# Kernel optimization log

Measured on AMD Instinct MI355X. Metric: run time of the kernel, lower is better.

## Reference

```python
import jax, jax.numpy as jnp
import numpy as np

N, B, D = 2048, 4, 2048   # seq_len, batch, embed_dim (sequence-first layout)
E = 2                     # expand_ratio
H = D // E                # number of heads
EPS = 1e-5


def setup_inputs() -> dict:
    key = jax.random.key(0)
    ks = jax.random.split(key, 3)
    x = jax.random.normal(ks[0], (N, B, D), dtype=jnp.float32)
    W_in = jax.random.normal(ks[1], (3 * D, D), dtype=jnp.float32) / np.sqrt(D).astype(np.float32)
    b_in = jnp.zeros((3 * D,), jnp.float32)
    W_out = jax.random.normal(ks[2], (D, D), dtype=jnp.float32) / np.sqrt(D).astype(np.float32)
    b_out = jnp.zeros((D,), jnp.float32)
    gamma = jnp.ones((D,), jnp.float32)
    beta = jnp.zeros((D,), jnp.float32)
    return {"x": x, "W_in": W_in, "b_in": b_in, "gamma": gamma, "beta": beta,
            "W_out": W_out, "b_out": b_out}


def _linear_scan(lam, u):
    # h_t = lam_t * h_{t-1} + u_t along time axis 0 (HgruRealFunction)
    def combine(c1, c2):
        a1, b1 = c1
        a2, b2 = c2
        return a1 * a2, a2 * b1 + b2
    _, h = jax.lax.associative_scan(combine, (lam, u), axis=0)
    return h


def _layernorm(x, gamma, beta):
    mu = jnp.mean(x, axis=-1, keepdims=True)
    var = jnp.var(x, axis=-1, keepdims=True)
    return (x - mu) * jax.lax.rsqrt(var + EPS) * gamma + beta


def reference(x, W_in, b_in, gamma, beta, W_out, b_out):
    n, b, d = x.shape
    feat = x @ W_in.T + b_in                       # (n,b,3d)
    inp, og, fg = jnp.split(feat, 3, axis=-1)
    inp = jax.nn.silu(inp)                         # act_fun = silu
    og = jax.nn.sigmoid(og)                        # uv_act_fun = sigmoid
    lam = jax.nn.sigmoid(fg)                       # lower_bound = 0 => lambda = sigmoid(F)

    inp = inp.reshape(n, b, H, E)
    og = og.reshape(n, b, H, E)
    lam = lam.reshape(n, b, H, E)

    # input = einsum('...hd,...he->...hde', 1-lambda, input)
    u = ((1.0 - lam)[..., :, None] * inp[..., None, :]).reshape(n, b, H * E * E)
    lam_f = jnp.broadcast_to(lam[..., :, None], (n, b, H, E, E)).reshape(n, b, H * E * E)

    s_fwd = _linear_scan(lam_f, u)
    s_rev = jnp.flip(_linear_scan(jnp.flip(lam_f, 0), jnp.flip(u, 0)), 0)
    s = (s_fwd + s_rev).reshape(n, b, H, E, E)

    o = jnp.einsum('nbhde,nbhd->nbhe', s, og).reshape(n, b, d)
    o = _layernorm(o, gamma, beta)
    return o @ W_out.T + b_out
```

## Files before the change

### kernel.cpp

```cpp
#include <hip/hip_runtime.h>
#include <hip/hip_bf16.h>

#define NSEQ 2048
#define NB   4
#define DIM  2048
#define HN   1024
#define FC   6144
#define MROWS 8192
#define CHUNKS 64
#define CLEN 32
#define NCH  4096

typedef __bf16 bf16x8_t __attribute__((ext_vector_type(8)));
typedef float  f32x4_t  __attribute__((ext_vector_type(4)));

__device__ __forceinline__ float sigm(float x){ return 1.f/(1.f + __expf(-x)); }
__device__ __forceinline__ float bflo(unsigned p){ return __uint_as_float(p << 16); }
__device__ __forceinline__ float bfhi(unsigned p){ return __uint_as_float(p & 0xffff0000u); }
__device__ __forceinline__ unsigned short f2bf(float f){
  union { __hip_bfloat16 h; unsigned short u; } cv;
  cv.h = __float2bfloat16(f);
  return cv.u;
}

__global__ __launch_bounds__(256) void cvt_bf16_4(const float4* __restrict__ in,
                                                  ushort4* __restrict__ out, int n4){
  int i = blockIdx.x * blockDim.x + threadIdx.x;
  int st = gridDim.x * blockDim.x;
  for (; i < n4; i += st){
    float4 v = in[i];
    ushort4 r;
    r.x = f2bf(v.x); r.y = f2bf(v.y); r.z = f2bf(v.z); r.w = f2bf(v.w);
    out[i] = r;
  }
}

__device__ __forceinline__ void gl_lds16(const void* g, void* l){
  __builtin_amdgcn_global_load_lds((const __attribute__((address_space(1))) void*)g,
                                   (__attribute__((address_space(3))) void*)l, 16, 0, 0);
}

template<int SLOT,int KSUB,int MH,bool VM, class SG>
__device__ __forceinline__ void do_phase(const __hip_bfloat16* smem,
    const int* aoff, const int* boff, bf16x8_t (&Bf)[4], f32x4_t (&acc)[8][4], SG&& sg){
  if (VM) asm volatile("s_waitcnt vmcnt(6)" ::: "memory");
  const __hip_bfloat16* base = smem + SLOT*32768 + KSUB*8192;
  bf16x8_t Af[4];
  #pragma unroll
  for (int mi = 0; mi < 4; ++mi)
    Af[mi] = *reinterpret_cast<const bf16x8_t*>(base + aoff[MH*4 + mi]);
  if (MH == 0){
    #pragma unroll
    for (int n = 0; n < 4; ++n)
      Bf[n] = *reinterpret_cast<const bf16x8_t*>(base + 16384 + boff[n]);
  }
  sg();
  __builtin_amdgcn_s_barrier();
  asm volatile("s_waitcnt lgkmcnt(0)" ::: "memory");
  __builtin_amdgcn_sched_barrier(0);
  __builtin_amdgcn_s_setprio(1);
  #pragma unroll
  for (int mi = 0; mi < 4; ++mi)
    #pragma unroll
    for (int n = 0; n < 4; ++n)
      acc[MH*4 + mi][n] =
        __builtin_amdgcn_mfma_f32_16x16x32_bf16(Af[mi], Bf[n], acc[MH*4 + mi][n], 0, 0, 0);
  __builtin_amdgcn_s_setprio(0);
  __builtin_amdgcn_s_barrier();
}

template <typename OutT>
__global__ __launch_bounds__(512, 2) void gemm256(const __hip_bfloat16* __restrict__ A,
                                                  const __hip_bfloat16* __restrict__ B,
                                                  const float* __restrict__ bias,
                                                  OutT* __restrict__ C,
                                                  int M, int N, int K, int nbx){
  __shared__ __align__(16) __hip_bfloat16 smem[65536];
  const int tid  = threadIdx.x;
  const int wave = tid >> 6, lane = tid & 63;

  const int cpx = gridDim.x >> 3;
  const int wg  = (blockIdx.x & 7) * cpx + (blockIdx.x >> 3);
  const int bx = wg % nbx, by = wg / nbx;
  const int m0 = by * 256, n0 = bx * 256;

  const int wr = wave >> 2, wc = wave & 3;
  const int r  = lane & 15, q = lane >> 4;
  const int NT = K >> 6;

  int aoff[8], boff[4];
  #pragma unroll
  for (int f = 0; f < 8; ++f){
    int R = wr*128 + (f>>2)*64 + (f&3)*16 + r;
    aoff[f] = (R>>1)*64 + (((((R&1)<<2) | q) ^ ((R>>1)&7)) << 3);
  }
  #pragma unroll
  for (int n = 0; n < 4; ++n){
    int R = wc*64 + n*16 + r;
    boff[n] = (R>>1)*64 + (((((R&1)<<2) | q) ^ ((R>>1)&7)) << 3);
  }

  auto stage_half = [&](int slot, int ab, int khalf, int ktile){
    if (ktile >= NT) return;
    const __hip_bfloat16* Base = ab ? B : A;
    const int t0 = ab ? n0 : m0;
    const int kc = ktile*64 + khalf*32;
    const int hb = slot*32768 + ab*16384 + khalf*8192;
    #pragma unroll
    for (int i = 0; i < 2; ++i){
      int g = i*512 + tid;
      int line = g >> 3, glp = g & 7;
      int glog = glp ^ (line & 7);
      int row = line*2 + (glog >> 2);
      int kg = glog & 3;
      gl_lds16(Base + (size_t)(t0 + row)*K + kc + kg*8, smem + hb + g*8);
    }
  };

  f32x4_t acc[8][4] = {};
  bf16x8_t Bf[4];

  stage_half(0,0,0, 0); stage_half(0,1,0, 0); stage_half(0,0,1, 0); stage_half(0,1,1, 0);
  stage_half(1,1,0, 1); stage_half(1,0,0, 1); stage_half(1,1,1, 1);
  asm volatile("s_waitcnt vmcnt(6)" ::: "memory");
  __builtin_amdgcn_s_barrier();

  for (int j = 0; j < NT/2; ++j){
    const int kb = 2*j;
    do_phase<0,0,0,true >(smem, aoff, boff, Bf, acc, [&]{ stage_half(1,0,1, kb+1); });
    do_phase<0,0,1,false>(smem, aoff, boff, Bf, acc, [&]{ stage_half(0,1,0, kb+2); });
    do_phase<0,1,0,true >(smem, aoff, boff, Bf, acc, [&]{ stage_half(0,0,0, kb+2); });
    do_phase<0,1,1,false>(smem, aoff, boff, Bf, acc, [&]{ stage_half(0,1,1, kb+2); });
    do_phase<1,0,0,true >(smem, aoff, boff, Bf, acc, [&]{ stage_half(0,0,1, kb+2); });
    do_phase<1,0,1,false>(smem, aoff, boff, Bf, acc, [&]{ stage_half(1,1,0, kb+3); });
    do_phase<1,1,0,true >(smem, aoff, boff, Bf, acc, [&]{ stage_half(1,0,0, kb+3); });
    do_phase<1,1,1,false>(smem, aoff, boff, Bf, acc, [&]{ stage_half(1,1,1, kb+3); });
  }

  #pragma unroll
  for (int fn = 0; fn < 4; ++fn){
    int col = n0 + wc*64 + fn*16 + r;
    float bv = bias[col];
    #pragma unroll
    for (int fm = 0; fm < 8; ++fm){
      int row0 = m0 + wr*128 + fm*16 + q*4;
      #pragma unroll
      for (int jj = 0; jj < 4; ++jj){
        float v = acc[fm][fn][jj] + bv;
        if constexpr (__is_same(OutT, float))
          C[(size_t)(row0 + jj)*N + col] = v;
        else
          C[(size_t)(row0 + jj)*N + col] = __float2bfloat16(v);
      }
    }
  }
}

struct SV { float l0, l1, u00, u01, u10, u11; };
__device__ __forceinline__ SV stepv(const unsigned* __restrict__ fp, int rowu){
  unsigned pi = fp[rowu];
  unsigned pf = fp[rowu + 2048];
  SV s;
  s.l0 = sigm(bflo(pf)); s.l1 = sigm(bfhi(pf));
  float i0 = bflo(pi), i1 = bfhi(pi);
  i0 *= sigm(i0); i1 *= sigm(i1);
  float a0 = 1.f - s.l0, a1 = 1.f - s.l1;
  s.u00 = a0*i0; s.u01 = a0*i1; s.u10 = a1*i0; s.u11 = a1*i1;
  return s;
}

__global__ __launch_bounds__(256) void scan_agg(const unsigned* __restrict__ feat,
    float* __restrict__ aggP, float4* __restrict__ aggHF, float4* __restrict__ aggHR){
  int ch = blockIdx.x*256 + threadIdx.x;
  int c  = blockIdx.y;
  int b = ch >> 10, h = ch & 1023;
  int base = b*3072 + h;
  int n0 = c*CLEN;
  float P0 = 1.f, P1 = 1.f;
  float f00=0,f01=0,f10=0,f11=0;
  for (int t = 0; t < CLEN; ++t){
    SV s = stepv(feat, (n0+t)*12288 + base);
    f00 = s.l0*f00 + s.u00; f01 = s.l0*f01 + s.u01;
    f10 = s.l1*f10 + s.u10; f11 = s.l1*f11 + s.u11;
    P0 *= s.l0; P1 *= s.l1;
  }
  float r00=0,r01=0,r10=0,r11=0;
  for (int t = CLEN-1; t >= 0; --t){
    SV s = stepv(feat, (n0+t)*12288 + base);
    r00 = s.l0*r00 + s.u00; r01 = s.l0*r01 + s.u01;
    r10 = s.l1*r10 + s.u10; r11 = s.l1*r11 + s.u11;
  }
  aggP[c*8192 + ch*2]     = P0;
  aggP[c*8192 + ch*2 + 1] = P1;
  aggHF[c*4096 + ch] = make_float4(f00,f01,f10,f11);
  aggHR[c*4096 + ch] = make_float4(r00,r01,r10,r11);
}

__global__ __launch_bounds__(256) void scan_carry(const float* __restrict__ aggP,
    const float* __restrict__ aggHF, const float* __restrict__ aggHR,
    float* __restrict__ cF, float* __restrict__ cR){
  int t  = blockIdx.x*256 + threadIdx.x;
  int pd = t >> 1;
  float s = 0.f;
  for (int c = 0; c < CHUNKS; ++c){
    cF[c*16384 + t] = s;
    s = aggP[c*8192 + pd]*s + aggHF[c*16384 + t];
  }
  s = 0.f;
  for (int c = CHUNKS-1; c >= 0; --c){
    cR[c*16384 + t] = s;
    s = aggP[c*8192 + pd]*s + aggHR[c*16384 + t];
  }
}

__global__ __launch_bounds__(256) void scan_fr(const unsigned* __restrict__ feat,
    const float4* __restrict__ cF, const float4* __restrict__ cR,
    float2* __restrict__ o){
  int ch = blockIdx.x*256 + threadIdx.x;
  int c  = blockIdx.y;
  int b = ch >> 10, h = ch & 1023;
  int base = b*3072 + h;
  float2 accv[CLEN];
  {
    float4 hv = cF[c*4096 + ch];
    float h00=hv.x, h01=hv.y, h10=hv.z, h11=hv.w;
    #pragma unroll
    for (int t = 0; t < CLEN; ++t){
      int rowu = (c*CLEN + t)*12288 + base;
      SV s = stepv(feat, rowu);
      h00 = s.l0*h00 + s.u00; h01 = s.l0*h01 + s.u01;
      h10 = s.l1*h10 + s.u10; h11 = s.l1*h11 + s.u11;
      unsigned po = feat[rowu + 1024];
      float g0 = sigm(bflo(po)), g1 = sigm(bfhi(po));
      accv[t] = make_float2(g0*h00 + g1*h10, g0*h01 + g1*h11);
    }
  }
  {
    float4 hv = cR[c*4096 + ch];
    float h00=hv.x, h01=hv.y, h10=hv.z, h11=hv.w;
    #pragma unroll
    for (int t = CLEN-1; t >= 0; --t){
      int rowu = (c*CLEN + t)*12288 + base;
      SV s = stepv(feat, rowu);
      h00 = s.l0*h00 + s.u00; h01 = s.l0*h01 + s.u01;
      h10 = s.l1*h10 + s.u10; h11 = s.l1*h11 + s.u11;
      unsigned po = feat[rowu + 1024];
      float g0 = sigm(bflo(po)), g1 = sigm(bfhi(po));
      accv[t].x += g0*h00 + g1*h10;
      accv[t].y += g0*h01 + g1*h11;
    }
  }
  #pragma unroll
  for (int t = 0; t < CLEN; ++t)
    o[((c*CLEN + t)*NB + b)*1024 + h] = accv[t];
}

__global__ __launch_bounds__(256) void layernorm_k(const float* __restrict__ o,
    const float* __restrict__ gamma, const float* __restrict__ beta,
    __hip_bfloat16* __restrict__ out){
  int row = blockIdx.x, t = threadIdx.x;
  const float4* x = (const float4*)(o + (size_t)row*DIM);
  float4 a = x[t], b = x[t + 256];
  float s  = (a.x + a.y) + (a.z + a.w) + (b.x + b.y) + (b.z + b.w);
  float ss = (a.x*a.x + a.y*a.y) + (a.z*a.z + a.w*a.w)
           + (b.x*b.x + b.y*b.y) + (b.z*b.z + b.w*b.w);
  #pragma unroll
  for (int off = 32; off > 0; off >>= 1){
    s  += __shfl_down(s, off);
    ss += __shfl_down(ss, off);
  }
  __shared__ float red[8];
  int wv = t >> 6, ln = t & 63;
  if (ln == 0){ red[wv] = s; red[4 + wv] = ss; }
  __syncthreads();
  float S  = (red[0] + red[1]) + (red[2] + red[3]);
  float SS = (red[4] + red[5]) + (red[6] + red[7]);
  float mu = S * (1.f/DIM);
  float rs = rsqrtf(SS * (1.f/DIM) - mu*mu + 1e-5f);
  const float4* gp = (const float4*)gamma;
  const float4* bp = (const float4*)beta;
  float4 g0 = gp[t], g1 = gp[t + 256], be0 = bp[t], be1 = bp[t + 256];
  ushort4* op = (ushort4*)(out + (size_t)row*DIM);
  ushort4 r0, r1;
  r0.x = f2bf((a.x - mu)*rs*g0.x + be0.x);
  r0.y = f2bf((a.y - mu)*rs*g0.y + be0.y);
  r0.z = f2bf((a.z - mu)*rs*g0.z + be0.z);
  r0.w = f2bf((a.w - mu)*rs*g0.w + be0.w);
  r1.x = f2bf((b.x - mu)*rs*g1.x + be1.x);
  r1.y = f2bf((b.y - mu)*rs*g1.y + be1.y);
  r1.z = f2bf((b.z - mu)*rs*g1.z + be1.z);
  r1.w = f2bf((b.w - mu)*rs*g1.w + be1.w);
  op[t] = r0; op[t + 256] = r1;
}

extern "C" void kernel_launch(void* const* d_in, const int* in_sizes, int n_in,
                              void* d_out, int out_size, void* d_ws, size_t ws_size,
                              hipStream_t stream){
  (void)in_sizes; (void)n_in; (void)out_size;
  const float* x     = (const float*)d_in[0];
  const float* W_in  = (const float*)d_in[1];
  const float* b_in  = (const float*)d_in[2];
  const float* gamma = (const float*)d_in[3];
  const float* beta  = (const float*)d_in[4];
  const float* W_out = (const float*)d_in[5];
  const float* b_out = (const float*)d_in[6];
  float* out = (float*)d_out;

  char* p = (char*)d_ws;
  auto carve = [&](size_t bytes) -> char* {
    char* r = p; p += (bytes + 255) & ~(size_t)255; return r;
  };
  __hip_bfloat16* feat = (__hip_bfloat16*)carve((size_t)MROWS*FC*2);
  char* U              = carve((size_t)MROWS*DIM*4);
  __hip_bfloat16* Wob  = (__hip_bfloat16*)carve((size_t)DIM*DIM*2);
  float* aggP  = (float*)carve((size_t)CHUNKS*8192*4);
  float* aggHF = (float*)carve((size_t)CHUNKS*16384*4);
  float* aggHR = (float*)carve((size_t)CHUNKS*16384*4);
  float* cF    = (float*)carve((size_t)CHUNKS*16384*4);
  float* cR    = (float*)carve((size_t)CHUNKS*16384*4);
  if ((size_t)(p - (char*)d_ws) > ws_size) return;

  __hip_bfloat16* xb  = (__hip_bfloat16*)U;
  __hip_bfloat16* Wib = (__hip_bfloat16*)(U + (size_t)MROWS*DIM*2);
  float* o            = (float*)U;
  __hip_bfloat16* oln = (__hip_bfloat16*)feat;

  cvt_bf16_4<<<2048, 256, 0, stream>>>((const float4*)x,     (ushort4*)xb,  MROWS*DIM/4);
  cvt_bf16_4<<<2048, 256, 0, stream>>>((const float4*)W_in,  (ushort4*)Wib, FC*DIM/4);
  cvt_bf16_4<<<1024, 256, 0, stream>>>((const float4*)W_out, (ushort4*)Wob, DIM*DIM/4);

  gemm256<__hip_bfloat16><<<768, 512, 0, stream>>>(xb, Wib, b_in, feat, MROWS, FC, 2048, FC/256);

  scan_agg  <<<dim3(NCH/256, CHUNKS), 256, 0, stream>>>((const unsigned*)feat, aggP, (float4*)aggHF, (float4*)aggHR);
  scan_carry<<<64, 256, 0, stream>>>(aggP, aggHF, aggHR, cF, cR);
  scan_fr   <<<dim3(NCH/256, CHUNKS), 256, 0, stream>>>((const unsigned*)feat, (const float4*)cF, (const float4*)cR, (float2*)o);

  layernorm_k<<<MROWS, 256, 0, stream>>>(o, gamma, beta, oln);

  gemm256<float><<<256, 512, 0, stream>>>(oln, Wob, b_out, out, MROWS, DIM, 2048, DIM/256);
}
```

Baseline: 479.8 us.

## Double-buffer LDS fragment reads to overlap with MFMA in GEMM phases

```diff
diff --git a/kernel.cpp b/kernel.cpp
--- a/kernel.cpp
+++ b/kernel.cpp
@@ -40,32 +40,35 @@
                                    (__attribute__((address_space(3))) void*)l, 16, 0, 0);
 }
 
-template<int SLOT,int KSUB,int MH,bool VM, class SG>
-__device__ __forceinline__ void do_phase(const __hip_bfloat16* smem,
-    const int* aoff, const int* boff, bf16x8_t (&Bf)[4], f32x4_t (&acc)[8][4], SG&& sg){
-  if (VM) asm volatile("s_waitcnt vmcnt(6)" ::: "memory");
-  const __hip_bfloat16* base = smem + SLOT*32768 + KSUB*8192;
-  bf16x8_t Af[4];
+template<int P, bool VM, class SG>
+__device__ __forceinline__ void phase(const __hip_bfloat16* smem,
+    const int (&aoff)[8], const int (&boff)[4],
+    bf16x8_t (&FA)[2][4], bf16x8_t (&FB)[2][4],
+    f32x4_t (&acc)[8][4], SG&& sg){
+  constexpr int Q  = (P+1)&7;
+  constexpr int qs = Q>>2, qk = (Q>>1)&1, qm = Q&1;
+  constexpr int mh = P&1;
+  constexpr int bs = (P>>1)&1;
+  const __hip_bfloat16* ab = smem + qs*32768 + qk*8192;
   #pragma unroll
   for (int mi = 0; mi < 4; ++mi)
-    Af[mi] = *reinterpret_cast<const bf16x8_t*>(base + aoff[MH*4 + mi]);
-  if (MH == 0){
+    FA[Q&1][mi] = *reinterpret_cast<const bf16x8_t*>(ab + aoff[qm*4 + mi]);
+  if (qm == 0){
+    const __hip_bfloat16* bb = smem + qs*32768 + 16384 + qk*8192;
     #pragma unroll
     for (int n = 0; n < 4; ++n)
-      Bf[n] = *reinterpret_cast<const bf16x8_t*>(base + 16384 + boff[n]);
+      FB[qk][n] = *reinterpret_cast<const bf16x8_t*>(bb + boff[n]);
   }
   sg();
-  __builtin_amdgcn_s_barrier();
-  asm volatile("s_waitcnt lgkmcnt(0)" ::: "memory");
-  __builtin_amdgcn_sched_barrier(0);
   __builtin_amdgcn_s_setprio(1);
   #pragma unroll
   for (int mi = 0; mi < 4; ++mi)
     #pragma unroll
     for (int n = 0; n < 4; ++n)
-      acc[MH*4 + mi][n] =
-        __builtin_amdgcn_mfma_f32_16x16x32_bf16(Af[mi], Bf[n], acc[MH*4 + mi][n], 0, 0, 0);
+      acc[mh*4 + mi][n] = __builtin_amdgcn_mfma_f32_16x16x32_bf16(
+          FA[P&1][mi], FB[bs][n], acc[mh*4 + mi][n], 0, 0, 0);
   __builtin_amdgcn_s_setprio(0);
+  if (VM) asm volatile("s_waitcnt vmcnt(8)" ::: "memory");
   __builtin_amdgcn_s_barrier();
 }
 
@@ -118,23 +121,34 @@
   };
 
   f32x4_t acc[8][4] = {};
-  bf16x8_t Bf[4];
-
-  stage_half(0,0,0, 0); stage_half(0,1,0, 0); stage_half(0,0,1, 0); stage_half(0,1,1, 0);
-  stage_half(1,1,0, 1); stage_half(1,0,0, 1); stage_half(1,1,1, 1);
-  asm volatile("s_waitcnt vmcnt(6)" ::: "memory");
+  bf16x8_t FA[2][4], FB[2][4];
+
+  stage_half(0,0,0, 0);
+  stage_half(0,1,0, 0);
+  stage_half(0,0,1, 0);
+  stage_half(0,1,1, 0);
+  stage_half(1,1,0, 1);
+  stage_half(1,0,0, 1);
+  stage_half(1,1,1, 1);
+  asm volatile("s_waitcnt vmcnt(10)" ::: "memory");
   __builtin_amdgcn_s_barrier();
+  #pragma unroll
+  for (int mi = 0; mi < 4; ++mi)
+    FA[0][mi] = *reinterpret_cast<const bf16x8_t*>(smem + aoff[mi]);
+  #pragma unroll
+  for (int n = 0; n < 4; ++n)
+    FB[0][n] = *reinterpret_cast<const bf16x8_t*>(smem + 16384 + boff[n]);
 
   for (int j = 0; j < NT/2; ++j){
     const int kb = 2*j;
-    do_phase<0,0,0,true >(smem, aoff, boff, Bf, acc, [&]{ stage_half(1,0,1, kb+1); });
-    do_phase<0,0,1,false>(smem, aoff, boff, Bf, acc, [&]{ stage_half(0,1,0, kb+2); });
-    do_phase<0,1,0,true >(smem, aoff, boff, Bf, acc, [&]{ stage_half(0,0,0, kb+2); });
-    do_phase<0,1,1,false>(smem, aoff, boff, Bf, acc, [&]{ stage_half(0,1,1, kb+2); });
-    do_phase<1,0,0,true >(smem, aoff, boff, Bf, acc, [&]{ stage_half(0,0,1, kb+2); });
-    do_phase<1,0,1,false>(smem, aoff, boff, Bf, acc, [&]{ stage_half(1,1,0, kb+3); });
-    do_phase<1,1,0,true >(smem, aoff, boff, Bf, acc, [&]{ stage_half(1,0,0, kb+3); });
-    do_phase<1,1,1,false>(smem, aoff, boff, Bf, acc, [&]{ stage_half(1,1,1, kb+3); });
+    phase<0,true >(smem, aoff, boff, FA, FB, acc, [&]{ stage_half(1,0,1, kb+1); });
+    phase<1,false>(smem, aoff, boff, FA, FB, acc, [&]{ stage_half(0,1,0, kb+2); });
+    phase<2,true >(smem, aoff, boff, FA, FB, acc, [&]{ stage_half(0,0,0, kb+2); });
+    phase<3,false>(smem, aoff, boff, FA, FB, acc, [&]{ stage_half(0,1,1, kb+2); });
+    phase<4,true >(smem, aoff, boff, FA, FB, acc, [&]{ stage_half(0,0,1, kb+2); });
+    phase<5,false>(smem, aoff, boff, FA, FB, acc, [&]{ stage_half(1,1,0, kb+3); });
+    phase<6,true >(smem, aoff, boff, FA, FB, acc, [&]{ stage_half(1,0,0, kb+3); });
+    phase<7,false>(smem, aoff, boff, FA, FB, acc, [&]{ stage_half(1,1,1, kb+3); });
   }
 
   #pragma unroll
```

Result: slower. 494.8 us (+3.1%).
